# Kernel tuning notes

Hardware: AMD Instinct MI355X
Metric: run time of the kernel (lower is better)

Reference implementation:

```python
import jax, jax.numpy as jnp
import numpy as np

B, P, D, H = 4, 2048, 768, 12  # batch, patches, patch_dims, heads
HD = D // H
EPS = 1e-5


def _layernorm(x, g, b):
    mu = jnp.mean(x, axis=-1, keepdims=True)
    var = jnp.mean(jnp.square(x - mu), axis=-1, keepdims=True)
    return (x - mu) * jax.lax.rsqrt(var + EPS) * g + b


def setup_inputs() -> dict:
    key = jax.random.key(0)
    ks = jax.random.split(key, 4)
    s = 0.02
    return {
        "x": jax.random.normal(ks[0], (B, P, D), jnp.float32),
        "ln1_w": jnp.ones((D,), jnp.float32),
        "ln1_b": jnp.zeros((D,), jnp.float32),
        "w_qkv": jax.random.normal(ks[1], (D, 3 * D), jnp.float32) * s,
        "b_qkv": jnp.zeros((3 * D,), jnp.float32),
        "ln2_w": jnp.ones((D,), jnp.float32),
        "ln2_b": jnp.zeros((D,), jnp.float32),
        "w_fc1": jax.random.normal(ks[2], (D, 4 * D), jnp.float32) * s,
        "b_fc1": jnp.zeros((4 * D,), jnp.float32),
        "w_fc2": jax.random.normal(ks[3], (4 * D, D), jnp.float32) * s,
        "b_fc2": jnp.zeros((D,), jnp.float32),
    }


def reference(x, ln1_w, ln1_b, w_qkv, b_qkv, ln2_w, ln2_b, w_fc1, b_fc1, w_fc2, b_fc2):
    scale = HD ** -0.5
    # --- attention block (pre-norm) ---
    residual = x
    h = _layernorm(x, ln1_w, ln1_b)
    qkv = h @ w_qkv + b_qkv                              # (B, P, 3D)
    qkv = qkv.reshape(B, P, 3, H, HD).transpose(2, 0, 3, 1, 4)  # (3, B, H, P, HD)
    q, k, v = qkv[0], qkv[1], qkv[2]
    attn = jnp.einsum('bhpd,bhqd->bhpq', q, k) * scale   # (B, H, P, P)
    # NOTE: original uses nn.Softmax(dim=1) -> normalizes over HEADS axis
    attn = jax.nn.softmax(attn, axis=1)
    out = jnp.einsum('bhpq,bhqd->bhpd', attn, v)         # (B, H, P, HD)
    out = out.transpose(0, 2, 1, 3).reshape(B, P, D)
    x = out + residual
    # --- MLP block (pre-norm) ---
    residual = x
    h = _layernorm(x, ln2_w, ln2_b)
    h = jax.nn.gelu(h @ w_fc1 + b_fc1, approximate=False)
    h = h @ w_fc2 + b_fc2
    return h + residual
```

## Files before the change

### kernel.cpp

```cpp
#include <hip/hip_runtime.h>
#include <hip/hip_bf16.h>

typedef __bf16 bf8 __attribute__((ext_vector_type(8)));
typedef float f4 __attribute__((ext_vector_type(4)));
typedef unsigned short u16;
typedef unsigned int u32;

#define B_ 4
#define P_ 2048
#define D_ 768
#define H_ 12
#define HD_ 64
#define EXPC_ 0.18033688011112042f

typedef const __attribute__((address_space(1))) void gvoid;
typedef __attribute__((address_space(3))) void lvoid;

__device__ __forceinline__ void gl_lds16(const u16* g, u16* l) {
  __builtin_amdgcn_global_load_lds((gvoid*)g, (lvoid*)l, 16, 0, 0);
}

__device__ __forceinline__ u16 f2bf(float f) {
  union { float f; u32 u; } c; c.f = f;
  u32 u = c.u;
  u += 0x7fffu + ((u >> 16) & 1u);
  return (u16)(u >> 16);
}

__device__ __forceinline__ float bf2f(u16 v) {
  union { u32 u; float f; } c; c.u = (u32)v << 16; return c.f;
}

__device__ __forceinline__ uint2 pack4(f4 v) {
  union { float f; u32 u; } a, b, c, d;
  a.f = v[0]; b.f = v[1]; c.f = v[2]; d.f = v[3];
  uint2 r;
  r.x = (a.u >> 16) | (b.u & 0xffff0000u);
  r.y = (c.u >> 16) | (d.u & 0xffff0000u);
  return r;
}

__device__ __forceinline__ f4 unpack4(ushort4 v) {
  f4 r;
  r[0] = bf2f(v.x); r[1] = bf2f(v.y); r[2] = bf2f(v.z); r[3] = bf2f(v.w);
  return r;
}

__device__ __forceinline__ f4 unp2(uint2 u) {
  f4 r;
  r[0] = bf2f((u16)(u.x & 0xffffu)); r[1] = bf2f((u16)(u.x >> 16));
  r[2] = bf2f((u16)(u.y & 0xffffu)); r[3] = bf2f((u16)(u.y >> 16));
  return r;
}

__device__ __forceinline__ bf8 mkbf8(f4 a, f4 b) {
  union { uint4 u; bf8 v; } c;
  uint2 l = pack4(a), h = pack4(b);
  c.u = make_uint4(l.x, l.y, h.x, h.y);
  return c.v;
}

__device__ __forceinline__ f4 mfma16(bf8 a, bf8 b, f4 c) {
  return __builtin_amdgcn_mfma_f32_16x16x32_bf16(a, b, c, 0, 0, 0);
}

#define ZERO44(acc)                    \
  {                                    \
    f4 z_ = {0.f, 0.f, 0.f, 0.f};      \
    for (int i_ = 0; i_ < 4; ++i_)     \
      for (int j_ = 0; j_ < 4; ++j_)   \
        acc[i_][j_] = z_;              \
  }

__device__ __forceinline__ int xcd_swz(int lin, int nwg) {
  return (lin & 7) * (nwg >> 3) + (lin >> 3);
}

__global__ __launch_bounds__(256) void tcast_k(const float* __restrict__ src,
                                               u16* __restrict__ dst, int R, int C) {
  __shared__ float t[32][33];
  int c0 = blockIdx.x * 32, r0 = blockIdx.y * 32;
  int tx = threadIdx.x & 31, ty = threadIdx.x >> 5;
  #pragma unroll
  for (int i = 0; i < 32; i += 8) {
    int r = r0 + ty + i, c = c0 + tx;
    t[ty + i][tx] = (r < R && c < C) ? src[(size_t)r * C + c] : 0.f;
  }
  __syncthreads();
  #pragma unroll
  for (int i = 0; i < 32; i += 8) {
    int c = c0 + ty + i, r = r0 + tx;
    if (c < C && r < R) dst[(size_t)c * R + r] = f2bf(t[tx][ty + i]);
  }
}

__global__ __launch_bounds__(256) void ln_k(const float* __restrict__ x,
                                            const float* __restrict__ g,
                                            const float* __restrict__ b,
                                            u16* __restrict__ out) {
  int row = blockIdx.x;
  const float* xr = x + (size_t)row * D_;
  float v0 = xr[threadIdx.x], v1 = xr[threadIdx.x + 256], v2 = xr[threadIdx.x + 512];
  float s = v0 + v1 + v2;
  float s2 = v0 * v0 + v1 * v1 + v2 * v2;
  #pragma unroll
  for (int o = 32; o > 0; o >>= 1) {
    s += __shfl_down(s, o, 64);
    s2 += __shfl_down(s2, o, 64);
  }
  __shared__ float a[4], a2[4];
  int wv = threadIdx.x >> 6;
  if ((threadIdx.x & 63) == 0) { a[wv] = s; a2[wv] = s2; }
  __syncthreads();
  s = a[0] + a[1] + a[2] + a[3];
  s2 = a2[0] + a2[1] + a2[2] + a2[3];
  float mean = s * (1.f / 768.f);
  float var = s2 * (1.f / 768.f) - mean * mean;
  float rstd = rsqrtf(var + 1e-5f);
  u16* orow = out + (size_t)row * D_;
  float vv[3] = {v0, v1, v2};
  #pragma unroll
  for (int j = 0; j < 3; ++j) {
    int i = threadIdx.x + j * 256;
    orow[i] = f2bf((vv[j] - mean) * rstd * g[i] + b[i]);
  }
}

__global__ __launch_bounds__(256) void ln2add_k(const float* __restrict__ x,
                                                const u16* __restrict__ O0,
                                                const u16* __restrict__ O1,
                                                const float* __restrict__ g,
                                                const float* __restrict__ b,
                                                float* __restrict__ x2,
                                                u16* __restrict__ out) {
  int row = blockIdx.x;
  const float* xr = x + (size_t)row * D_;
  const u16* o0 = O0 + (size_t)row * D_;
  const u16* o1 = O1 + (size_t)row * D_;
  float vv[3];
  #pragma unroll
  for (int j = 0; j < 3; ++j) {
    int i = threadIdx.x + j * 256;
    vv[j] = xr[i] + bf2f(o0[i]) + bf2f(o1[i]);
  }
  float s = vv[0] + vv[1] + vv[2];
  float s2 = vv[0] * vv[0] + vv[1] * vv[1] + vv[2] * vv[2];
  #pragma unroll
  for (int o = 32; o > 0; o >>= 1) {
    s += __shfl_down(s, o, 64);
    s2 += __shfl_down(s2, o, 64);
  }
  __shared__ float a[4], a2[4];
  int wv = threadIdx.x >> 6;
  if ((threadIdx.x & 63) == 0) { a[wv] = s; a2[wv] = s2; }
  __syncthreads();
  s = a[0] + a[1] + a[2] + a[3];
  s2 = a2[0] + a2[1] + a2[2] + a2[3];
  float mean = s * (1.f / 768.f);
  float var = s2 * (1.f / 768.f) - mean * mean;
  float rstd = rsqrtf(var + 1e-5f);
  float* x2r = x2 + (size_t)row * D_;
  u16* orow = out + (size_t)row * D_;
  #pragma unroll
  for (int j = 0; j < 3; ++j) {
    int i = threadIdx.x + j * 256;
    x2r[i] = vv[j];
    orow[i] = f2bf((vv[j] - mean) * rstd * g[i] + b[i]);
  }
}

template <int K>
__device__ __forceinline__ void staged_core(const u16* __restrict__ Ab,
                                            const u16* __restrict__ Bb,
                                            u16* As, u16* Bs, f4 acc[4][4]) {
  const int wave = threadIdx.x >> 6, lane = threadIdx.x & 63;
  const int l15 = lane & 15, quad = lane >> 4;
  const int lrow = lane >> 2;
  const int lcol = (lane & 3) * 8;
  const int mw = (wave & 1) * 64, nw = (wave >> 1) * 64;
  for (int k0 = 0; k0 < K; k0 += 32) {
    const u16* ga = Ab + (size_t)(wave * 32 + lrow) * K + k0 + lcol;
    gl_lds16(ga, &As[(wave * 32) * 32]);
    gl_lds16(ga + (size_t)16 * K, &As[(wave * 32 + 16) * 32]);
    const u16* gb = Bb + (size_t)(wave * 32 + lrow) * K + k0 + lcol;
    gl_lds16(gb, &Bs[(wave * 32) * 32]);
    gl_lds16(gb + (size_t)16 * K, &Bs[(wave * 32 + 16) * 32]);
    __syncthreads();
    bf8 a[4], b[4];
    #pragma unroll
    for (int mt = 0; mt < 4; ++mt)
      a[mt] = *reinterpret_cast<const bf8*>(&As[(mw + mt * 16 + l15) * 32 + quad * 8]);
    #pragma unroll
    for (int nt = 0; nt < 4; ++nt)
      b[nt] = *reinterpret_cast<const bf8*>(&Bs[(nw + nt * 16 + l15) * 32 + quad * 8]);
    __builtin_amdgcn_s_setprio(1);
    #pragma unroll
    for (int mt = 0; mt < 4; ++mt)
      #pragma unroll
      for (int nt = 0; nt < 4; ++nt)
        acc[mt][nt] = mfma16(a[mt], b[nt], acc[mt][nt]);
    __builtin_amdgcn_s_setprio(0);
    __syncthreads();
  }
}

__global__ __launch_bounds__(256) void gemm_qkv_k(const u16* __restrict__ hln,
                                                  const u16* __restrict__ wT,
                                                  const float* __restrict__ bias,
                                                  u16* __restrict__ Q, u16* __restrict__ Km,
                                                  u16* __restrict__ Vt) {
  __shared__ u16 As[128 * 32], Bs[128 * 32];
  int lin = blockIdx.y * gridDim.x + blockIdx.x;
  int swz = xcd_swz(lin, gridDim.x * gridDim.y);
  int m0 = (swz / gridDim.x) * 128, n0 = (swz % gridDim.x) * 128;
  f4 acc[4][4];
  ZERO44(acc);
  staged_core<768>(hln + (size_t)m0 * 768, wT + (size_t)n0 * 768, As, Bs, acc);
  int wave = threadIdx.x >> 6, lane = threadIdx.x & 63, l15 = lane & 15, quad = lane >> 4;
  int mW = m0 + (wave & 1) * 64, nW = n0 + (wave >> 1) * 64;
  #pragma unroll
  for (int mt = 0; mt < 4; ++mt)
    #pragma unroll
    for (int nt = 0; nt < 4; ++nt)
      #pragma unroll
      for (int r = 0; r < 4; ++r) {
        int m = mW + mt * 16 + quad * 4 + r;
        int n = nW + nt * 16 + l15;
        float v = acc[mt][nt][r] + bias[n];
        u16 bv = f2bf(v);
        int b = m >> 11, p = m & 2047;
        int which = n / 768, hn = n % 768;
        int h = hn >> 6, d = hn & 63;
        if (which == 0)
          Q[((size_t)(b * H_ + h) * P_ + p) * HD_ + d] = bv;
        else if (which == 1)
          Km[((size_t)(b * H_ + h) * P_ + p) * HD_ + d] = bv;
        else
          Vt[((size_t)(b * H_ + h) * HD_ + d) * P_ + p] = bv;
      }
}

__global__ __launch_bounds__(256) void gemm_fc1_k(const u16* __restrict__ A,
                                                  const u16* __restrict__ wT,
                                                  const float* __restrict__ bias,
                                                  u16* __restrict__ out) {
  __shared__ u16 As[128 * 32], Bs[128 * 32];
  int lin = blockIdx.y * gridDim.x + blockIdx.x;
  int swz = xcd_swz(lin, gridDim.x * gridDim.y);
  int m0 = (swz / gridDim.x) * 128, n0 = (swz % gridDim.x) * 128;
  f4 acc[4][4];
  ZERO44(acc);
  staged_core<768>(A + (size_t)m0 * 768, wT + (size_t)n0 * 768, As, Bs, acc);
  int wave = threadIdx.x >> 6, lane = threadIdx.x & 63, l15 = lane & 15, quad = lane >> 4;
  int mW = m0 + (wave & 1) * 64, nW = n0 + (wave >> 1) * 64;
  #pragma unroll
  for (int mt = 0; mt < 4; ++mt)
    #pragma unroll
    for (int nt = 0; nt < 4; ++nt)
      #pragma unroll
      for (int r = 0; r < 4; ++r) {
        int m = mW + mt * 16 + quad * 4 + r;
        int n = nW + nt * 16 + l15;
        float v = acc[mt][nt][r] + bias[n];
        v = 0.5f * v * (1.f + erff(v * 0.70710678f));
        out[(size_t)m * 3072 + n] = f2bf(v);
      }
}

__global__ __launch_bounds__(256) void gemm_fc2_k(const u16* __restrict__ A,
                                                  const u16* __restrict__ wT,
                                                  const float* __restrict__ bias,
                                                  const float* __restrict__ resid,
                                                  float* __restrict__ out) {
  __shared__ u16 As[128 * 32], Bs[64 * 32];
  int wave = threadIdx.x >> 6, lane = threadIdx.x & 63, l15 = lane & 15, quad = lane >> 4;
  int lrow = lane >> 2, lcol = (lane & 3) * 8;
  int lin = blockIdx.y * gridDim.x + blockIdx.x;
  int swz = xcd_swz(lin, gridDim.x * gridDim.y);
  int m0 = (swz / gridDim.x) * 128, n0 = (swz % gridDim.x) * 64;
  const u16* Ab = A + (size_t)m0 * 3072;
  const u16* Bb = wT + (size_t)n0 * 3072;
  int mw = (wave & 1) * 64, nw = (wave >> 1) * 32;
  f4 acc[4][2];
  #pragma unroll
  for (int i = 0; i < 4; ++i)
    #pragma unroll
    for (int j = 0; j < 2; ++j) acc[i][j] = f4{0.f, 0.f, 0.f, 0.f};
  for (int k0 = 0; k0 < 3072; k0 += 32) {
    const u16* ga = Ab + (size_t)(wave * 32 + lrow) * 3072 + k0 + lcol;
    gl_lds16(ga, &As[(wave * 32) * 32]);
    gl_lds16(ga + (size_t)16 * 3072, &As[(wave * 32 + 16) * 32]);
    const u16* gb = Bb + (size_t)(wave * 16 + lrow) * 3072 + k0 + lcol;
    gl_lds16(gb, &Bs[(wave * 16) * 32]);
    __syncthreads();
    bf8 a[4], b[2];
    #pragma unroll
    for (int mt = 0; mt < 4; ++mt)
      a[mt] = *reinterpret_cast<const bf8*>(&As[(mw + mt * 16 + l15) * 32 + quad * 8]);
    #pragma unroll
    for (int nt = 0; nt < 2; ++nt)
      b[nt] = *reinterpret_cast<const bf8*>(&Bs[(nw + nt * 16 + l15) * 32 + quad * 8]);
    __builtin_amdgcn_s_setprio(1);
    #pragma unroll
    for (int mt = 0; mt < 4; ++mt)
      #pragma unroll
      for (int nt = 0; nt < 2; ++nt)
        acc[mt][nt] = mfma16(a[mt], b[nt], acc[mt][nt]);
    __builtin_amdgcn_s_setprio(0);
    __syncthreads();
  }
  int mW = m0 + mw, nW = n0 + nw;
  #pragma unroll
  for (int mt = 0; mt < 4; ++mt)
    #pragma unroll
    for (int nt = 0; nt < 2; ++nt)
      #pragma unroll
      for (int r = 0; r < 4; ++r) {
        int m = mW + mt * 16 + quad * 4 + r;
        int n = nW + nt * 16 + l15;
        size_t idx = (size_t)m * 768 + n;
        out[idx] = acc[mt][nt][r] + bias[n] + resid[idx];
      }
}

__global__ __launch_bounds__(768) void attn_fused_k(const u16* __restrict__ Q,
                                                    const u16* __restrict__ Km,
                                                    const u16* __restrict__ Vt,
                                                    u16* __restrict__ O0,
                                                    u16* __restrict__ O1) {
  int id = blockIdx.x;
  int g = id & 7, pt = id >> 3;
  int b = g >> 1, qs = g & 1;
  int w = threadIdx.x >> 6, lane = threadIdx.x & 63, l15 = lane & 15, quad = lane >> 4;
  __shared__ __align__(16) u16 E[12][64][36];
  __shared__ __align__(16) float R[64][36];

  const u16* Qp = Q + ((size_t)(b * H_ + w) * P_ + pt * 64) * HD_;
  const u16* Kbase = Km + ((size_t)(b * H_ + w) * P_ + qs * 1024) * HD_;
  const u16* Vbase = Vt + (size_t)(b * H_ + w) * HD_ * P_ + qs * 1024;

  bf8 qf[4][2];
  #pragma unroll
  for (int nt = 0; nt < 4; ++nt)
    #pragma unroll
    for (int ks = 0; ks < 2; ++ks)
      qf[nt][ks] = *reinterpret_cast<const bf8*>(Qp + (size_t)(nt * 16 + l15) * HD_ + ks * 32 + quad * 8);

  f4 oacc[4][4];
  ZERO44(oacc);

  for (int qt = 0; qt < 32; ++qt) {
    const u16* Kp = Kbase + (size_t)qt * 32 * HD_;
    bf8 kf[2][2];
    #pragma unroll
    for (int mt = 0; mt < 2; ++mt)
      #pragma unroll
      for (int ks = 0; ks < 2; ++ks)
        kf[mt][ks] = *reinterpret_cast<const bf8*>(Kp + (size_t)(mt * 16 + l15) * HD_ + ks * 32 + quad * 8);
    bf8 vf[4];
    #pragma unroll
    for (int dt = 0; dt < 4; ++dt)
      vf[dt] = *reinterpret_cast<const bf8*>(Vbase + (size_t)(dt * 16 + l15) * P_ + qt * 32 + quad * 8);
    #pragma unroll
    for (int mt = 0; mt < 2; ++mt) {
      f4 s[4];
      #pragma unroll
      for (int nt = 0; nt < 4; ++nt) s[nt] = f4{0.f, 0.f, 0.f, 0.f};
      __builtin_amdgcn_s_setprio(1);
      #pragma unroll
      for (int nt = 0; nt < 4; ++nt) {
        s[nt] = mfma16(kf[mt][0], qf[nt][0], s[nt]);
        s[nt] = mfma16(kf[mt][1], qf[nt][1], s[nt]);
      }
      __builtin_amdgcn_s_setprio(0);
      #pragma unroll
      for (int nt = 0; nt < 4; ++nt) {
        f4 e;
        #pragma unroll
        for (int r = 0; r < 4; ++r) e[r] = __builtin_amdgcn_exp2f(s[nt][r] * EXPC_);
        *reinterpret_cast<uint2*>(&E[w][nt * 16 + l15][mt * 16 + quad * 4]) = pack4(e);
      }
    }
    __syncthreads();
    if (threadIdx.x < 512) {
      int p = threadIdx.x >> 3, qc = (threadIdx.x & 7) * 4;
      f4 sum = {0.f, 0.f, 0.f, 0.f};
      #pragma unroll
      for (int h = 0; h < 12; ++h)
        sum += unpack4(*reinterpret_cast<const ushort4*>(&E[h][p][qc]));
      f4 rc;
      #pragma unroll
      for (int c = 0; c < 4; ++c) rc[c] = __builtin_amdgcn_rcpf(sum[c]);
      *reinterpret_cast<f4*>(&R[p][qc]) = rc;
    }
    __syncthreads();
    #pragma unroll
    for (int pi = 0; pi < 4; ++pi) {
      int pp = pi * 16 + l15;
      uint2 e0 = *reinterpret_cast<const uint2*>(&E[w][pp][quad * 8]);
      uint2 e1 = *reinterpret_cast<const uint2*>(&E[w][pp][quad * 8 + 4]);
      f4 r0 = *reinterpret_cast<const f4*>(&R[pp][quad * 8]);
      f4 r1 = *reinterpret_cast<const f4*>(&R[pp][quad * 8 + 4]);
      bf8 af = mkbf8(unp2(e0) * r0, unp2(e1) * r1);
      __builtin_amdgcn_s_setprio(1);
      #pragma unroll
      for (int dt = 0; dt < 4; ++dt)
        oacc[dt][pi] = mfma16(vf[dt], af, oacc[dt][pi]);
      __builtin_amdgcn_s_setprio(0);
    }
  }
  __syncthreads();
  u16(*Os)[64][72] = reinterpret_cast<u16(*)[64][72]>(&E[0][0][0]);
  u16* Op = qs ? O1 : O0;
  #pragma unroll
  for (int hh = 0; hh < 2; ++hh) {
    if (w >= hh * 6 && w < hh * 6 + 6) {
      int wp = w - hh * 6;
      #pragma unroll
      for (int dt = 0; dt < 4; ++dt)
        #pragma unroll
        for (int pi = 0; pi < 4; ++pi)
          *reinterpret_cast<uint2*>(&Os[wp][pi * 16 + l15][dt * 16 + quad * 4]) = pack4(oacc[dt][pi]);
    }
    __syncthreads();
    #pragma unroll
    for (int j = 0; j < 4; ++j) {
      int c = threadIdx.x + j * 768;
      int p = c / 48, m = c % 48;
      int hp = m >> 3, d = (m & 7) * 8;
      uint4 val = *reinterpret_cast<const uint4*>(&Os[hp][p][d]);
      size_t go = (((size_t)b * P_) + pt * 64 + p) * D_ + (hh * 6 + hp) * 64 + d;
      *reinterpret_cast<uint4*>(Op + go) = val;
    }
    __syncthreads();
  }
}

extern "C" void kernel_launch(void* const* d_in, const int* in_sizes, int n_in,
                              void* d_out, int out_size, void* d_ws, size_t ws_size,
                              hipStream_t stream) {
  const float* x = (const float*)d_in[0];
  const float* ln1w = (const float*)d_in[1];
  const float* ln1b = (const float*)d_in[2];
  const float* wqkv = (const float*)d_in[3];
  const float* bqkv = (const float*)d_in[4];
  const float* ln2w = (const float*)d_in[5];
  const float* ln2b = (const float*)d_in[6];
  const float* wfc1 = (const float*)d_in[7];
  const float* bfc1 = (const float*)d_in[8];
  const float* wfc2 = (const float*)d_in[9];
  const float* bfc2 = (const float*)d_in[10];
  float* out = (float*)d_out;

  char* ws = (char*)d_ws;
  size_t off = 0;
  auto alloc = [&](size_t bytes) -> void* {
    void* p = ws + off;
    off += (bytes + 255) & ~(size_t)255;
    return p;
  };
  u16* hln = (u16*)alloc((size_t)8192 * 768 * 2);
  u16* wqkvT = (u16*)alloc((size_t)2304 * 768 * 2);
  u16* wfc1T = (u16*)alloc((size_t)3072 * 768 * 2);
  u16* wfc2T = (u16*)alloc((size_t)768 * 3072 * 2);
  u16* Qb = (u16*)alloc((size_t)B_ * H_ * P_ * HD_ * 2);
  u16* Kb = (u16*)alloc((size_t)B_ * H_ * P_ * HD_ * 2);
  u16* Vtb = (u16*)alloc((size_t)B_ * H_ * HD_ * P_ * 2);
  float* x2 = (float*)alloc((size_t)8192 * 768 * 4);
  u16* O0 = (u16*)alloc((size_t)8192 * 768 * 2);
  u16* O1 = (u16*)alloc((size_t)8192 * 768 * 2);
  u16* gbuf = (u16*)alloc((size_t)8192 * 3072 * 2);

  tcast_k<<<dim3(72, 24), 256, 0, stream>>>(wqkv, wqkvT, 768, 2304);
  tcast_k<<<dim3(96, 24), 256, 0, stream>>>(wfc1, wfc1T, 768, 3072);
  tcast_k<<<dim3(24, 96), 256, 0, stream>>>(wfc2, wfc2T, 3072, 768);
  ln_k<<<8192, 256, 0, stream>>>(x, ln1w, ln1b, hln);
  gemm_qkv_k<<<dim3(18, 64), 256, 0, stream>>>(hln, wqkvT, bqkv, Qb, Kb, Vtb);
  attn_fused_k<<<256, 768, 0, stream>>>(Qb, Kb, Vtb, O0, O1);
  ln2add_k<<<8192, 256, 0, stream>>>(x, O0, O1, ln2w, ln2b, x2, hln);
  gemm_fc1_k<<<dim3(24, 64), 256, 0, stream>>>(hln, wfc1T, bfc1, gbuf);
  gemm_fc2_k<<<dim3(12, 64), 256, 0, stream>>>(gbuf, wfc2T, bfc2, x2, out);
}
```

Baseline: 480.3 us.

## Split fused attention into head-softmax denominator kernel and per-head PV kernel

The single fused attention kernel becomes two. The first recomputes QK^T for all 12 heads, accumulates the cross-head exp sums with shared-memory atomics, and writes reciprocal denominators to a global B×P×P float buffer. The second recomputes QK^T per head group with smaller 256-thread blocks and more blocks, multiplies the exps by those denominators, and runs the PV matmul. The aim is more parallelism and better occupancy than the 256 large blocks with per-tile block syncs. The cost is computing QK^T twice and writing then reading a 64 MB reciprocal buffer.

```diff
diff --git a/kernel.cpp b/kernel.cpp
--- a/kernel.cpp
+++ b/kernel.cpp
@@ -37,12 +37,6 @@
   uint2 r;
   r.x = (a.u >> 16) | (b.u & 0xffff0000u);
   r.y = (c.u >> 16) | (d.u & 0xffff0000u);
-  return r;
-}
-
-__device__ __forceinline__ f4 unpack4(ushort4 v) {
-  f4 r;
-  r[0] = bf2f(v.x); r[1] = bf2f(v.y); r[2] = bf2f(v.z); r[3] = bf2f(v.w);
   return r;
 }
 
@@ -323,21 +317,21 @@
       }
 }
 
-__global__ __launch_bounds__(768) void attn_fused_k(const u16* __restrict__ Q,
-                                                    const u16* __restrict__ Km,
-                                                    const u16* __restrict__ Vt,
-                                                    u16* __restrict__ O0,
-                                                    u16* __restrict__ O1) {
-  int id = blockIdx.x;
-  int g = id & 7, pt = id >> 3;
-  int b = g >> 1, qs = g & 1;
+__global__ __launch_bounds__(768) void denom_k(const u16* __restrict__ Q,
+                                               const u16* __restrict__ Km,
+                                               float* __restrict__ Rg) {
+  int xg = blockIdx.x & 7, r = blockIdx.x >> 3;
+  int g = xg + 8 * (r & 1);
+  int pt = r >> 1;
+  int b = g >> 2, qq = g & 3;
   int w = threadIdx.x >> 6, lane = threadIdx.x & 63, l15 = lane & 15, quad = lane >> 4;
-  __shared__ __align__(16) u16 E[12][64][36];
-  __shared__ __align__(16) float R[64][36];
+  __shared__ float Dsh[64][67];
+
+  for (int i = threadIdx.x; i < 64 * 67; i += 768) (&Dsh[0][0])[i] = 0.f;
+  __syncthreads();
 
   const u16* Qp = Q + ((size_t)(b * H_ + w) * P_ + pt * 64) * HD_;
-  const u16* Kbase = Km + ((size_t)(b * H_ + w) * P_ + qs * 1024) * HD_;
-  const u16* Vbase = Vt + (size_t)(b * H_ + w) * HD_ * P_ + qs * 1024;
+  const u16* Kbase = Km + ((size_t)(b * H_ + w) * P_ + qq * 512) * HD_;
 
   bf8 qf[4][2];
   #pragma unroll
@@ -346,93 +340,153 @@
     for (int ks = 0; ks < 2; ++ks)
       qf[nt][ks] = *reinterpret_cast<const bf8*>(Qp + (size_t)(nt * 16 + l15) * HD_ + ks * 32 + quad * 8);
 
-  f4 oacc[4][4];
-  ZERO44(oacc);
-
-  for (int qt = 0; qt < 32; ++qt) {
-    const u16* Kp = Kbase + (size_t)qt * 32 * HD_;
-    bf8 kf[2][2];
-    #pragma unroll
-    for (int mt = 0; mt < 2; ++mt)
-      #pragma unroll
-      for (int ks = 0; ks < 2; ++ks)
-        kf[mt][ks] = *reinterpret_cast<const bf8*>(Kp + (size_t)(mt * 16 + l15) * HD_ + ks * 32 + quad * 8);
-    bf8 vf[4];
-    #pragma unroll
-    for (int dt = 0; dt < 4; ++dt)
-      vf[dt] = *reinterpret_cast<const bf8*>(Vbase + (size_t)(dt * 16 + l15) * P_ + qt * 32 + quad * 8);
-    #pragma unroll
-    for (int mt = 0; mt < 2; ++mt) {
+  for (int t = 0; t < 8; ++t) {
+    const u16* Kp = Kbase + (size_t)t * 64 * HD_;
+    #pragma unroll
+    for (int mt = 0; mt < 4; ++mt) {
+      bf8 kfa = *reinterpret_cast<const bf8*>(Kp + (size_t)(mt * 16 + l15) * HD_ + quad * 8);
+      bf8 kfb = *reinterpret_cast<const bf8*>(Kp + (size_t)(mt * 16 + l15) * HD_ + 32 + quad * 8);
       f4 s[4];
       #pragma unroll
       for (int nt = 0; nt < 4; ++nt) s[nt] = f4{0.f, 0.f, 0.f, 0.f};
       __builtin_amdgcn_s_setprio(1);
       #pragma unroll
       for (int nt = 0; nt < 4; ++nt) {
-        s[nt] = mfma16(kf[mt][0], qf[nt][0], s[nt]);
-        s[nt] = mfma16(kf[mt][1], qf[nt][1], s[nt]);
+        s[nt] = mfma16(kfa, qf[nt][0], s[nt]);
+        s[nt] = mfma16(kfb, qf[nt][1], s[nt]);
       }
       __builtin_amdgcn_s_setprio(0);
       #pragma unroll
       for (int nt = 0; nt < 4; ++nt) {
-        f4 e;
         #pragma unroll
-        for (int r = 0; r < 4; ++r) e[r] = __builtin_amdgcn_exp2f(s[nt][r] * EXPC_);
-        *reinterpret_cast<uint2*>(&E[w][nt * 16 + l15][mt * 16 + quad * 4]) = pack4(e);
+        for (int rr = 0; rr < 4; ++rr) {
+          float e = __builtin_amdgcn_exp2f(s[nt][rr] * EXPC_);
+          atomicAdd(&Dsh[nt * 16 + l15][mt * 16 + quad * 4 + rr], e);
+        }
       }
     }
     __syncthreads();
-    if (threadIdx.x < 512) {
-      int p = threadIdx.x >> 3, qc = (threadIdx.x & 7) * 4;
-      f4 sum = {0.f, 0.f, 0.f, 0.f};
-      #pragma unroll
-      for (int h = 0; h < 12; ++h)
-        sum += unpack4(*reinterpret_cast<const ushort4*>(&E[h][p][qc]));
+    float* Rw = Rg + ((size_t)(b * P_ + pt * 64)) * P_ + qq * 512 + t * 64;
+    for (int c = threadIdx.x; c < 1024; c += 768) {
+      int p = c >> 4, qc = (c & 15) * 4;
       f4 rc;
       #pragma unroll
-      for (int c = 0; c < 4; ++c) rc[c] = __builtin_amdgcn_rcpf(sum[c]);
-      *reinterpret_cast<f4*>(&R[p][qc]) = rc;
+      for (int i = 0; i < 4; ++i) {
+        rc[i] = __builtin_amdgcn_rcpf(Dsh[p][qc + i]);
+        Dsh[p][qc + i] = 0.f;
+      }
+      *reinterpret_cast<f4*>(Rw + (size_t)p * P_ + qc) = rc;
     }
     __syncthreads();
-    #pragma unroll
-    for (int pi = 0; pi < 4; ++pi) {
-      int pp = pi * 16 + l15;
-      uint2 e0 = *reinterpret_cast<const uint2*>(&E[w][pp][quad * 8]);
-      uint2 e1 = *reinterpret_cast<const uint2*>(&E[w][pp][quad * 8 + 4]);
-      f4 r0 = *reinterpret_cast<const f4*>(&R[pp][quad * 8]);
-      f4 r1 = *reinterpret_cast<const f4*>(&R[pp][quad * 8 + 4]);
-      bf8 af = mkbf8(unp2(e0) * r0, unp2(e1) * r1);
-      __builtin_amdgcn_s_setprio(1);
+  }
+}
+
+__global__ __launch_bounds__(256) void pv_k(const u16* __restrict__ Q,
+                                            const u16* __restrict__ Km,
+                                            const u16* __restrict__ Vt,
+                                            const float* __restrict__ Rg,
+                                            u16* __restrict__ O0,
+                                            u16* __restrict__ O1) {
+  __shared__ __align__(16) u16 smem[4 * 32 * 68];
+  int xg = blockIdx.x & 7, r = blockIdx.x >> 3;
+  int b = xg >> 1, qs = xg & 1;
+  int hg = r % 3, pt = r / 3;
+  int w = threadIdx.x >> 6, lane = threadIdx.x & 63, l15 = lane & 15, quad = lane >> 4;
+  int h = hg * 4 + w;
+  u16* Ew = smem + w * 32 * 68;
+
+  const u16* Qp = Q + ((size_t)(b * H_ + h) * P_ + pt * 32) * HD_;
+  const u16* Kbase = Km + ((size_t)(b * H_ + h) * P_ + qs * 1024) * HD_;
+  const u16* Vbase = Vt + (size_t)(b * H_ + h) * HD_ * P_ + qs * 1024;
+  const float* Rbase = Rg + ((size_t)(b * P_ + pt * 32)) * P_ + qs * 1024;
+
+  bf8 qf[2][2];
+  #pragma unroll
+  for (int nt = 0; nt < 2; ++nt)
+    #pragma unroll
+    for (int ks = 0; ks < 2; ++ks)
+      qf[nt][ks] = *reinterpret_cast<const bf8*>(Qp + (size_t)(nt * 16 + l15) * HD_ + ks * 32 + quad * 8);
+
+  f4 oacc[4][2];
+  #pragma unroll
+  for (int i = 0; i < 4; ++i)
+    #pragma unroll
+    for (int j = 0; j < 2; ++j) oacc[i][j] = f4{0.f, 0.f, 0.f, 0.f};
+
+  for (int t = 0; t < 16; ++t) {
+    const u16* Kp = Kbase + (size_t)t * 64 * HD_;
+    #pragma unroll
+    for (int mth = 0; mth < 2; ++mth) {
+      bf8 kf[2][2];
+      #pragma unroll
+      for (int i = 0; i < 2; ++i)
+        #pragma unroll
+        for (int ks = 0; ks < 2; ++ks)
+          kf[i][ks] = *reinterpret_cast<const bf8*>(
+              Kp + (size_t)((mth * 2 + i) * 16 + l15) * HD_ + ks * 32 + quad * 8);
+      #pragma unroll
+      for (int i = 0; i < 2; ++i) {
+        int mt = mth * 2 + i;
+        f4 s[2];
+        #pragma unroll
+        for (int nt = 0; nt < 2; ++nt) s[nt] = f4{0.f, 0.f, 0.f, 0.f};
+        __builtin_amdgcn_s_setprio(1);
+        #pragma unroll
+        for (int nt = 0; nt < 2; ++nt) {
+          s[nt] = mfma16(kf[i][0], qf[nt][0], s[nt]);
+          s[nt] = mfma16(kf[i][1], qf[nt][1], s[nt]);
+        }
+        __builtin_amdgcn_s_setprio(0);
+        #pragma unroll
+        for (int nt = 0; nt < 2; ++nt) {
+          f4 e;
+          #pragma unroll
+          for (int rr = 0; rr < 4; ++rr) e[rr] = __builtin_amdgcn_exp2f(s[nt][rr] * EXPC_);
+          *reinterpret_cast<uint2*>(&Ew[(nt * 16 + l15) * 68 + mt * 16 + quad * 4]) = pack4(e);
+        }
+      }
+    }
+    #pragma unroll
+    for (int half = 0; half < 2; ++half) {
+      int bq = t * 64 + half * 32;
+      bf8 vf[4];
       #pragma unroll
       for (int dt = 0; dt < 4; ++dt)
-        oacc[dt][pi] = mfma16(vf[dt], af, oacc[dt][pi]);
-      __builtin_amdgcn_s_setprio(0);
+        vf[dt] = *reinterpret_cast<const bf8*>(Vbase + (size_t)(dt * 16 + l15) * P_ + bq + quad * 8);
+      #pragma unroll
+      for (int pi = 0; pi < 2; ++pi) {
+        int pp = pi * 16 + l15;
+        uint2 e0 = *reinterpret_cast<const uint2*>(&Ew[pp * 68 + half * 32 + quad * 8]);
+        uint2 e1 = *reinterpret_cast<const uint2*>(&Ew[pp * 68 + half * 32 + quad * 8 + 4]);
+        const float* Rr = Rbase + (size_t)pp * P_ + bq + quad * 8;
+        f4 r0 = *reinterpret_cast<const f4*>(Rr);
+        f4 r1 = *reinterpret_cast<const f4*>(Rr + 4);
+        bf8 af = mkbf8(unp2(e0) * r0, unp2(e1) * r1);
+        __builtin_amdgcn_s_setprio(1);
+        #pragma unroll
+        for (int dt = 0; dt < 4; ++dt)
+          oacc[dt][pi] = mfma16(vf[dt], af, oacc[dt][pi]);
+        __builtin_amdgcn_s_setprio(0);
+      }
     }
   }
   __syncthreads();
-  u16(*Os)[64][72] = reinterpret_cast<u16(*)[64][72]>(&E[0][0][0]);
+  #pragma unroll
+  for (int dt = 0; dt < 4; ++dt)
+    #pragma unroll
+    for (int pi = 0; pi < 2; ++pi)
+      *reinterpret_cast<uint2*>(&smem[(pi * 16 + l15) * 272 + w * 68 + dt * 16 + quad * 4]) =
+          pack4(oacc[dt][pi]);
+  __syncthreads();
   u16* Op = qs ? O1 : O0;
   #pragma unroll
-  for (int hh = 0; hh < 2; ++hh) {
-    if (w >= hh * 6 && w < hh * 6 + 6) {
-      int wp = w - hh * 6;
-      #pragma unroll
-      for (int dt = 0; dt < 4; ++dt)
-        #pragma unroll
-        for (int pi = 0; pi < 4; ++pi)
-          *reinterpret_cast<uint2*>(&Os[wp][pi * 16 + l15][dt * 16 + quad * 4]) = pack4(oacc[dt][pi]);
-    }
-    __syncthreads();
-    #pragma unroll
-    for (int j = 0; j < 4; ++j) {
-      int c = threadIdx.x + j * 768;
-      int p = c / 48, m = c % 48;
-      int hp = m >> 3, d = (m & 7) * 8;
-      uint4 val = *reinterpret_cast<const uint4*>(&Os[hp][p][d]);
-      size_t go = (((size_t)b * P_) + pt * 64 + p) * D_ + (hh * 6 + hp) * 64 + d;
-      *reinterpret_cast<uint4*>(Op + go) = val;
-    }
-    __syncthreads();
+  for (int j = 0; j < 8; ++j) {
+    int c = threadIdx.x + j * 256;
+    int p = c >> 6, cw = c & 63;
+    int hp = cw >> 4, dq = (cw & 15) * 4;
+    uint2 val = *reinterpret_cast<const uint2*>(&smem[p * 272 + hp * 68 + dq]);
+    size_t row = (size_t)b * P_ + pt * 32 + p;
+    *reinterpret_cast<uint2*>(Op + row * D_ + hg * 256 + hp * 64 + dq) = val;
   }
 }
 
@@ -470,13 +524,15 @@
   u16* O0 = (u16*)alloc((size_t)8192 * 768 * 2);
   u16* O1 = (u16*)alloc((size_t)8192 * 768 * 2);
   u16* gbuf = (u16*)alloc((size_t)8192 * 3072 * 2);
+  float* Rg = (float*)alloc((size_t)B_ * P_ * P_ * 4);
 
   tcast_k<<<dim3(72, 24), 256, 0, stream>>>(wqkv, wqkvT, 768, 2304);
   tcast_k<<<dim3(96, 24), 256, 0, stream>>>(wfc1, wfc1T, 768, 3072);
   tcast_k<<<dim3(24, 96), 256, 0, stream>>>(wfc2, wfc2T, 3072, 768);
   ln_k<<<8192, 256, 0, stream>>>(x, ln1w, ln1b, hln);
   gemm_qkv_k<<<dim3(18, 64), 256, 0, stream>>>(hln, wqkvT, bqkv, Qb, Kb, Vtb);
-  attn_fused_k<<<256, 768, 0, stream>>>(Qb, Kb, Vtb, O0, O1);
+  denom_k<<<512, 768, 0, stream>>>(Qb, Kb, Rg);
+  pv_k<<<1536, 256, 0, stream>>>(Qb, Kb, Vtb, Rg, O0, O1);
   ln2add_k<<<8192, 256, 0, stream>>>(x, O0, O1, ln2w, ln2b, x2, hln);
   gemm_fc1_k<<<dim3(24, 64), 256, 0, stream>>>(hln, wfc1T, bfc1, gbuf);
   gemm_fc2_k<<<dim3(12, 64), 256, 0, stream>>>(gbuf, wfc2T, bfc2, x2, out);
```

After: 1.609 ms. +235.0%, slower.

## Split attention into smaller 256-thread blocks with waves covering three heads

Applied to the files above, without the earlier changes.

Restructures the fused attention kernel from 256 blocks of 12 waves (one head per wave, 64 query rows) into 1024 blocks of 4 waves, each wave handling three heads over 16 query rows. The aim is finer-grained scheduling, smaller LDS footprint per block and cheaper block-wide barriers. The trade-off is that K and V tiles are re-read four times as often across blocks, adding L2 traffic, and V loads move after the barrier.

```diff
diff --git a/kernel.cpp b/kernel.cpp
--- a/kernel.cpp
+++ b/kernel.cpp
@@ -323,66 +323,61 @@
       }
 }
 
-__global__ __launch_bounds__(768) void attn_fused_k(const u16* __restrict__ Q,
-                                                    const u16* __restrict__ Km,
-                                                    const u16* __restrict__ Vt,
-                                                    u16* __restrict__ O0,
-                                                    u16* __restrict__ O1) {
+__global__ __launch_bounds__(256) void attn_k(const u16* __restrict__ Q,
+                                              const u16* __restrict__ Km,
+                                              const u16* __restrict__ Vt,
+                                              u16* __restrict__ O0,
+                                              u16* __restrict__ O1) {
+  __shared__ __align__(16) u16 E[12][16][36];
+  __shared__ __align__(16) float R[16][36];
+
   int id = blockIdx.x;
   int g = id & 7, pt = id >> 3;
   int b = g >> 1, qs = g & 1;
   int w = threadIdx.x >> 6, lane = threadIdx.x & 63, l15 = lane & 15, quad = lane >> 4;
-  __shared__ __align__(16) u16 E[12][64][36];
-  __shared__ __align__(16) float R[64][36];
-
-  const u16* Qp = Q + ((size_t)(b * H_ + w) * P_ + pt * 64) * HD_;
-  const u16* Kbase = Km + ((size_t)(b * H_ + w) * P_ + qs * 1024) * HD_;
-  const u16* Vbase = Vt + (size_t)(b * H_ + w) * HD_ * P_ + qs * 1024;
-
-  bf8 qf[4][2];
-  #pragma unroll
-  for (int nt = 0; nt < 4; ++nt)
+
+  bf8 qf[3][2];
+  #pragma unroll
+  for (int hi = 0; hi < 3; ++hi) {
+    int h = w + 4 * hi;
+    const u16* Qp = Q + ((size_t)(b * H_ + h) * P_ + pt * 16) * HD_;
     #pragma unroll
     for (int ks = 0; ks < 2; ++ks)
-      qf[nt][ks] = *reinterpret_cast<const bf8*>(Qp + (size_t)(nt * 16 + l15) * HD_ + ks * 32 + quad * 8);
-
-  f4 oacc[4][4];
-  ZERO44(oacc);
+      qf[hi][ks] = *reinterpret_cast<const bf8*>(Qp + (size_t)l15 * HD_ + ks * 32 + quad * 8);
+  }
+
+  f4 oacc[3][4];
+  #pragma unroll
+  for (int i = 0; i < 3; ++i)
+    #pragma unroll
+    for (int j = 0; j < 4; ++j) oacc[i][j] = f4{0.f, 0.f, 0.f, 0.f};
 
   for (int qt = 0; qt < 32; ++qt) {
-    const u16* Kp = Kbase + (size_t)qt * 32 * HD_;
-    bf8 kf[2][2];
-    #pragma unroll
-    for (int mt = 0; mt < 2; ++mt)
-      #pragma unroll
-      for (int ks = 0; ks < 2; ++ks)
-        kf[mt][ks] = *reinterpret_cast<const bf8*>(Kp + (size_t)(mt * 16 + l15) * HD_ + ks * 32 + quad * 8);
-    bf8 vf[4];
-    #pragma unroll
-    for (int dt = 0; dt < 4; ++dt)
-      vf[dt] = *reinterpret_cast<const bf8*>(Vbase + (size_t)(dt * 16 + l15) * P_ + qt * 32 + quad * 8);
-    #pragma unroll
-    for (int mt = 0; mt < 2; ++mt) {
-      f4 s[4];
-      #pragma unroll
-      for (int nt = 0; nt < 4; ++nt) s[nt] = f4{0.f, 0.f, 0.f, 0.f};
-      __builtin_amdgcn_s_setprio(1);
-      #pragma unroll
-      for (int nt = 0; nt < 4; ++nt) {
-        s[nt] = mfma16(kf[mt][0], qf[nt][0], s[nt]);
-        s[nt] = mfma16(kf[mt][1], qf[nt][1], s[nt]);
-      }
-      __builtin_amdgcn_s_setprio(0);
-      #pragma unroll
-      for (int nt = 0; nt < 4; ++nt) {
+    #pragma unroll
+    for (int hi = 0; hi < 3; ++hi) {
+      int h = w + 4 * hi;
+      const u16* Kp = Km + ((size_t)(b * H_ + h) * P_ + qs * 1024 + qt * 32) * HD_;
+      bf8 kf[2][2];
+      #pragma unroll
+      for (int mt = 0; mt < 2; ++mt)
+        #pragma unroll
+        for (int ks = 0; ks < 2; ++ks)
+          kf[mt][ks] = *reinterpret_cast<const bf8*>(Kp + (size_t)(mt * 16 + l15) * HD_ + ks * 32 + quad * 8);
+      #pragma unroll
+      for (int mt = 0; mt < 2; ++mt) {
+        f4 s = {0.f, 0.f, 0.f, 0.f};
+        __builtin_amdgcn_s_setprio(1);
+        s = mfma16(kf[mt][0], qf[hi][0], s);
+        s = mfma16(kf[mt][1], qf[hi][1], s);
+        __builtin_amdgcn_s_setprio(0);
         f4 e;
         #pragma unroll
-        for (int r = 0; r < 4; ++r) e[r] = __builtin_amdgcn_exp2f(s[nt][r] * EXPC_);
-        *reinterpret_cast<uint2*>(&E[w][nt * 16 + l15][mt * 16 + quad * 4]) = pack4(e);
+        for (int r = 0; r < 4; ++r) e[r] = __builtin_amdgcn_exp2f(s[r] * EXPC_);
+        *reinterpret_cast<uint2*>(&E[h][l15][mt * 16 + quad * 4]) = pack4(e);
       }
     }
     __syncthreads();
-    if (threadIdx.x < 512) {
+    if (threadIdx.x < 128) {
       int p = threadIdx.x >> 3, qc = (threadIdx.x & 7) * 4;
       f4 sum = {0.f, 0.f, 0.f, 0.f};
       #pragma unroll
@@ -395,41 +390,48 @@
     }
     __syncthreads();
     #pragma unroll
-    for (int pi = 0; pi < 4; ++pi) {
-      int pp = pi * 16 + l15;
-      uint2 e0 = *reinterpret_cast<const uint2*>(&E[w][pp][quad * 8]);
-      uint2 e1 = *reinterpret_cast<const uint2*>(&E[w][pp][quad * 8 + 4]);
-      f4 r0 = *reinterpret_cast<const f4*>(&R[pp][quad * 8]);
-      f4 r1 = *reinterpret_cast<const f4*>(&R[pp][quad * 8 + 4]);
+    for (int hi = 0; hi < 3; ++hi) {
+      int h = w + 4 * hi;
+      const u16* Vp = Vt + (size_t)(b * H_ + h) * HD_ * P_ + qs * 1024 + qt * 32;
+      bf8 vf[4];
+      #pragma unroll
+      for (int dt = 0; dt < 4; ++dt)
+        vf[dt] = *reinterpret_cast<const bf8*>(Vp + (size_t)(dt * 16 + l15) * P_ + quad * 8);
+      uint2 e0 = *reinterpret_cast<const uint2*>(&E[h][l15][quad * 8]);
+      uint2 e1 = *reinterpret_cast<const uint2*>(&E[h][l15][quad * 8 + 4]);
+      f4 r0 = *reinterpret_cast<const f4*>(&R[l15][quad * 8]);
+      f4 r1 = *reinterpret_cast<const f4*>(&R[l15][quad * 8 + 4]);
       bf8 af = mkbf8(unp2(e0) * r0, unp2(e1) * r1);
       __builtin_amdgcn_s_setprio(1);
       #pragma unroll
       for (int dt = 0; dt < 4; ++dt)
-        oacc[dt][pi] = mfma16(vf[dt], af, oacc[dt][pi]);
+        oacc[hi][dt] = mfma16(vf[dt], af, oacc[hi][dt]);
       __builtin_amdgcn_s_setprio(0);
     }
   }
   __syncthreads();
-  u16(*Os)[64][72] = reinterpret_cast<u16(*)[64][72]>(&E[0][0][0]);
+  u16(*Os)[16][72] = reinterpret_cast<u16(*)[16][72]>(&E[0][0][0]);
   u16* Op = qs ? O1 : O0;
   #pragma unroll
   for (int hh = 0; hh < 2; ++hh) {
-    if (w >= hh * 6 && w < hh * 6 + 6) {
-      int wp = w - hh * 6;
-      #pragma unroll
-      for (int dt = 0; dt < 4; ++dt)
+    #pragma unroll
+    for (int hi = 0; hi < 3; ++hi) {
+      int h = w + 4 * hi;
+      if (h >= hh * 6 && h < hh * 6 + 6) {
+        int hp = h - hh * 6;
         #pragma unroll
-        for (int pi = 0; pi < 4; ++pi)
-          *reinterpret_cast<uint2*>(&Os[wp][pi * 16 + l15][dt * 16 + quad * 4]) = pack4(oacc[dt][pi]);
+        for (int dt = 0; dt < 4; ++dt)
+          *reinterpret_cast<uint2*>(&Os[hp][l15][dt * 16 + quad * 4]) = pack4(oacc[hi][dt]);
+      }
     }
     __syncthreads();
     #pragma unroll
-    for (int j = 0; j < 4; ++j) {
-      int c = threadIdx.x + j * 768;
+    for (int j = 0; j < 3; ++j) {
+      int c = threadIdx.x + j * 256;
       int p = c / 48, m = c % 48;
       int hp = m >> 3, d = (m & 7) * 8;
       uint4 val = *reinterpret_cast<const uint4*>(&Os[hp][p][d]);
-      size_t go = (((size_t)b * P_) + pt * 64 + p) * D_ + (hh * 6 + hp) * 64 + d;
+      size_t go = ((size_t)b * P_ + pt * 16 + p) * D_ + (hh * 6 + hp) * 64 + d;
       *reinterpret_cast<uint4*>(Op + go) = val;
     }
     __syncthreads();
@@ -476,7 +478,7 @@
   tcast_k<<<dim3(24, 96), 256, 0, stream>>>(wfc2, wfc2T, 3072, 768);
   ln_k<<<8192, 256, 0, stream>>>(x, ln1w, ln1b, hln);
   gemm_qkv_k<<<dim3(18, 64), 256, 0, stream>>>(hln, wqkvT, bqkv, Qb, Kb, Vtb);
-  attn_fused_k<<<256, 768, 0, stream>>>(Qb, Kb, Vtb, O0, O1);
+  attn_k<<<1024, 256, 0, stream>>>(Qb, Kb, Vtb, O0, O1);
   ln2add_k<<<8192, 256, 0, stream>>>(x, O0, O1, ln2w, ln2b, x2, hln);
   gemm_fc1_k<<<dim3(24, 64), 256, 0, stream>>>(hln, wfc1T, bfc1, gbuf);
   gemm_fc2_k<<<dim3(12, 64), 256, 0, stream>>>(gbuf, wfc2T, bfc2, x2, out);
```

After: 725.2 us. +51.0%, slower.
